# Optimization experiments

Hardware: AMD Instinct MI355X
Metric: run time of the kernel (lower is better)

Reference implementation:

```python
import jax, jax.numpy as jnp
import numpy as np

EPS = 0.05
ITERS = 10


def setup_inputs() -> dict:
    key = jax.random.key(0)
    k1, k2, k3 = jax.random.split(key, 3)
    x = jax.random.normal(k1, (32, 768, 32, 32), jnp.float32)          # [B,C,H,W]
    conv_w = jax.random.normal(k2, (384, 768), jnp.float32) * 0.02     # 1x1 conv kernel [D,C]
    conv_b = jnp.zeros((384,), jnp.float32)
    v = jax.random.normal(k3, (64, 384), jnp.float32)                  # cluster codebook [K,D]
    return {"x": x, "conv_w": conv_w, "conv_b": conv_b, "v": v}


def log_sinkhorn_iterations(Z, log_mu, log_nu, iters):
    # Z: [B,M,N]; log_mu: [B,M]; log_nu: [B,N]
    u0 = jnp.zeros_like(log_mu)
    v0 = jnp.zeros_like(log_nu)

    def step(carry, _):
        u, v = carry
        u = log_mu - jax.nn.logsumexp(Z + v[:, None, :], axis=2)
        v = log_nu - jax.nn.logsumexp(Z + u[:, :, None], axis=1)
        return (u, v), None

    (u, v), _ = jax.lax.scan(step, (u0, v0), None, length=iters)
    return Z + u[:, :, None] + v[:, None, :]


def log_optimal_transport(scores, eps, iters):
    b, m, n = scores.shape
    norm = -jnp.log(jnp.asarray(float(m + n), scores.dtype))
    log_mu = jnp.full((b, m), norm, scores.dtype)
    log_nu = jnp.full((b, n), norm, scores.dtype)
    Z = log_sinkhorn_iterations(scores / eps, log_mu, log_nu, iters)
    return jnp.exp(Z - norm)


def reference(x, conv_w, conv_b, v):
    b, c, h, w = x.shape
    d = conv_w.shape[0]
    # 1x1 conv projection, then flatten spatial and move channels last: [B, HW, D]
    x_proj = jnp.einsum('bchw,dc->bhwd', x, conv_w).reshape(b, h * w, d) + conv_b
    # l2_normalize tokens
    xn = x_proj / jnp.maximum(jnp.linalg.norm(x_proj, axis=-1, keepdims=True), 1e-12)
    # normalized cluster codebook (torch does this under no_grad + in-place copy)
    clusters = v / jnp.maximum(jnp.linalg.norm(v, axis=-1, keepdims=True), 1e-12)  # [K,D]
    # cluster scores: [B, HW, K]
    scores = jnp.einsum('bnd,kd->bnk', xn, clusters)
    # OT on transposed scores [B,K,HW], transpose weights back to [B,HW,K]
    weights = jnp.transpose(
        log_optimal_transport(jnp.transpose(scores, (0, 2, 1)), EPS, ITERS), (0, 2, 1))
    # v_tilde = (x^T @ weights)^T : [B, K, D]
    v_tilde = jnp.einsum('bnd,bnk->bkd', xn, weights)
    return (v_tilde, x_proj)
```

## Files before the change

kernel.cpp:

```cpp
#include <hip/hip_runtime.h>
#include <math.h>

#define BB 32
#define CC 768
#define HWN 1024
#define DD 384
#define KK 64
#define EPSI 20.0f
#define NORMC (-6.9920964f)
#define NITERS 10

typedef __bf16 bf16;
typedef bf16 bf16x8 __attribute__((ext_vector_type(8)));
typedef bf16 bf16x4 __attribute__((ext_vector_type(4)));
typedef float f32x4 __attribute__((ext_vector_type(4)));
typedef _Float16 f16;
typedef f16 f16x2 __attribute__((ext_vector_type(2)));
typedef f16 f16x4 __attribute__((ext_vector_type(4)));

__device__ __forceinline__ float wave_sum(float v){
  #pragma unroll
  for (int off = 32; off; off >>= 1) v += __shfl_xor(v, off, 64);
  return v;
}
__device__ __forceinline__ float wave_max(float v){
  #pragma unroll
  for (int off = 32; off; off >>= 1) v = fmaxf(v, __shfl_xor(v, off, 64));
  return v;
}

__device__ __forceinline__ void async16(const bf16* g, bf16* l){
  __builtin_amdgcn_global_load_lds((const __attribute__((address_space(1))) unsigned int*)g,
                                   (__attribute__((address_space(3))) unsigned int*)l,
                                   16, 0, 0);
}

__global__ __launch_bounds__(256) void k0_clusters(const float* __restrict__ vin,
                                                   bf16* __restrict__ clusb){
  int w = threadIdx.x >> 6, l = threadIdx.x & 63;
  int k = blockIdx.x * 4 + w;
  float s = 0.f;
  #pragma unroll
  for (int i = 0; i < 6; i++){ float x = vin[k*DD + l + 64*i]; s += x*x; }
  s = wave_sum(s);
  float scale = 1.f / fmaxf(sqrtf(s), 1e-12f);
  #pragma unroll
  for (int i = 0; i < 6; i++) clusb[k*DD + l + 64*i] = (bf16)(vin[k*DD + l + 64*i] * scale);
}

__global__ __launch_bounds__(256) void k_wconv(const float* __restrict__ w,
                                               bf16* __restrict__ wb){
  int i = (blockIdx.x * 256 + threadIdx.x) * 4;
  float4 v = *(const float4*)&w[i];
  bf16x4 o;
  o[0] = (bf16)v.x; o[1] = (bf16)v.y; o[2] = (bf16)v.z; o[3] = (bf16)v.w;
  *(bf16x4*)&wb[i] = o;
}

__global__ __launch_bounds__(256) void k_xt(const float* __restrict__ x,
                                            bf16* __restrict__ xt){
  __shared__ float S[64][68];
  int b  = blockIdx.z;
  int k0 = blockIdx.y * 64;
  int n0 = blockIdx.x * 64;
  const float* X = x + (size_t)b * CC * HWN;
  int t = threadIdx.x;
  int rr = t >> 4, cc = (t & 15) * 4;
  #pragma unroll
  for (int it = 0; it < 4; it++){
    float4 v = *(const float4*)&X[(size_t)(k0 + rr + it*16)*HWN + n0 + cc];
    *(float4*)&S[rr + it*16][cc] = v;
  }
  __syncthreads();
  int n = t >> 2, kc = t & 3;
  bf16* orow = xt + (size_t)b * HWN * CC + (size_t)(n0 + n) * CC + k0;
  #pragma unroll
  for (int half = 0; half < 2; half++){
    int kb = half*32 + kc*8;
    bf16x8 o;
    #pragma unroll
    for (int jj = 0; jj < 8; jj++){
      int j = (jj + kc) & 7;
      o[j] = (bf16)S[kb + j][n];
    }
    *(bf16x8*)&orow[kb] = o;
  }
}

__global__ __launch_bounds__(512) void k_gemm(const bf16* __restrict__ Wb,
                                              const bf16* __restrict__ Xt,
                                              const float* __restrict__ bias,
                                              float* __restrict__ xp){
  __shared__ bf16 Wl[384][4][8];
  __shared__ bf16 Xl[128][4][8];
  int b  = blockIdx.y;
  int n0 = blockIdx.x * 128;
  int t = threadIdx.x, wv = t >> 6, l = t & 63;
  int l15 = l & 15, quad = l >> 4;
  int wn = wv >> 2, wm = wv & 3;
  const bf16* Xb = Xt + (size_t)b * HWN * CC;

  int rbase = wv*16 + (l >> 2);
  int kq8   = (l & 3) * 8;
  const bf16* gX = Xb + (size_t)(n0 + rbase) * CC + kq8;
  const bf16* gW = Wb + (size_t)rbase * CC + kq8;
  bf16* lX = &Xl[0][0][0] + wv * 512;
  bf16* lW = &Wl[0][0][0] + wv * 512;

  f32x4 acc[4][6];
  const f32x4 zero = {0.f, 0.f, 0.f, 0.f};
  #pragma unroll
  for (int i = 0; i < 4; i++)
    #pragma unroll
    for (int j = 0; j < 6; j++) acc[i][j] = zero;

  for (int k0 = 0; k0 < CC; k0 += 32){
    async16(gX + k0, lX);
    async16(gW + k0,                  lW);
    async16(gW + k0 + (size_t)128*CC, lW + 4096);
    async16(gW + k0 + (size_t)256*CC, lW + 8192);
    __syncthreads();
    bf16x8 xf[4], wf[6];
    #pragma unroll
    for (int i = 0; i < 4; i++)
      xf[i] = *(const bf16x8*)&Xl[wn*64 + i*16 + l15][quad][0];
    #pragma unroll
    for (int j = 0; j < 6; j++)
      wf[j] = *(const bf16x8*)&Wl[wm*96 + j*16 + l15][quad][0];
    #pragma unroll
    for (int i = 0; i < 4; i++)
      #pragma unroll
      for (int j = 0; j < 6; j++)
        acc[i][j] = __builtin_amdgcn_mfma_f32_16x16x32_bf16(xf[i], wf[j], acc[i][j], 0, 0, 0);
    __syncthreads();
  }

  float bb[6];
  #pragma unroll
  for (int j = 0; j < 6; j++) bb[j] = bias[wm*96 + j*16 + l15];
  #pragma unroll
  for (int i = 0; i < 4; i++){
    int nb = n0 + wn*64 + i*16 + quad*4;
    #pragma unroll
    for (int r = 0; r < 4; r++){
      float* orow = xp + ((size_t)b * HWN + nb + r) * DD;
      #pragma unroll
      for (int j = 0; j < 6; j++)
        orow[wm*96 + j*16 + l15] = acc[i][j][r] + bb[j];
    }
  }
}

__global__ __launch_bounds__(256) void k2_rnorm(const float* __restrict__ xp,
                                                float* __restrict__ rn){
  int w = threadIdx.x >> 6, l = threadIdx.x & 63;
  int t = blockIdx.x * 4 + w;
  const float* row = xp + (size_t)t * DD;
  float s = 0.f;
  #pragma unroll
  for (int i = 0; i < 6; i++){ float xv = row[l + 64*i]; s += xv*xv; }
  s = wave_sum(s);
  if (l == 0) rn[t] = 1.f / fmaxf(sqrtf(s), 1e-12f);
}

__global__ __launch_bounds__(256) void k_xpt(const float* __restrict__ xp,
                                             const float* __restrict__ rn,
                                             bf16* __restrict__ xpt,
                                             bf16* __restrict__ xnb){
  __shared__ float S[64][68];
  int b  = blockIdx.z;
  int d0 = blockIdx.y * 64;
  int n0 = blockIdx.x * 64;
  const float* xpb = xp + (size_t)b * HWN * DD;
  const float* rnb = rn + (size_t)b * HWN;
  int t = threadIdx.x;
  int rr = t >> 4, cc = (t & 15) * 4;
  #pragma unroll
  for (int it = 0; it < 4; it++){
    int row = rr + it*16;
    float sc = rnb[n0 + row];
    float4 v = *(const float4*)&xpb[(size_t)(n0 + row)*DD + d0 + cc];
    v.x *= sc; v.y *= sc; v.z *= sc; v.w *= sc;
    *(float4*)&S[row][cc] = v;
    bf16x4 o4;
    o4[0] = (bf16)v.x; o4[1] = (bf16)v.y; o4[2] = (bf16)v.z; o4[3] = (bf16)v.w;
    *(bf16x4*)&xnb[((size_t)b * HWN + n0 + row)*DD + d0 + cc] = o4;
  }
  __syncthreads();
  int d = t >> 2, c0 = (t & 3) * 16;
  bf16* orow = xpt + (size_t)b * DD * HWN + (size_t)(d0 + d) * HWN + n0 + c0;
  bf16x8 o0, o1;
  #pragma unroll
  for (int jj = 0; jj < 8; jj++) o0[jj] = (bf16)S[c0 + jj][d];
  #pragma unroll
  for (int jj = 0; jj < 8; jj++) o1[jj] = (bf16)S[c0 + 8 + jj][d];
  *(bf16x8*)&orow[0] = o0;
  *(bf16x8*)&orow[8] = o1;
}

__global__ __launch_bounds__(256) void k3_scores(const bf16* __restrict__ clusb,
                                                 const bf16* __restrict__ xnb,
                                                 float* __restrict__ Z){
  __shared__ bf16 Al[64][4][8];
  __shared__ bf16 Bl[128][4][8];
  int b = blockIdx.y, n0 = blockIdx.x * 128;
  const bf16* Xb = xnb + (size_t)b * HWN * DD;
  int t = threadIdx.x, wv = t >> 6, l = t & 63;
  int l15 = l & 15, quad = l >> 4;

  int rbase = wv*16 + (l >> 2);
  int kq8   = (l & 3) * 8;
  const bf16* gA = clusb + (size_t)rbase * DD + kq8;
  const bf16* gB = Xb + (size_t)(n0 + rbase) * DD + kq8;
  bf16* lA = &Al[0][0][0] + wv * 512;
  bf16* lB = &Bl[0][0][0] + wv * 512;

  f32x4 acc[4][2];
  const f32x4 zero = {0.f, 0.f, 0.f, 0.f};
  #pragma unroll
  for (int i = 0; i < 4; i++){ acc[i][0] = zero; acc[i][1] = zero; }

  for (int d0 = 0; d0 < DD; d0 += 32){
    async16(gA + d0, lA);
    async16(gB + d0,                 lB);
    async16(gB + d0 + (size_t)64*DD, lB + 2048);
    __syncthreads();
    bf16x8 af[4], bf[2];
    #pragma unroll
    for (int i = 0; i < 4; i++)
      af[i] = *(const bf16x8*)&Al[i*16 + l15][quad][0];
    #pragma unroll
    for (int j = 0; j < 2; j++)
      bf[j] = *(const bf16x8*)&Bl[wv*32 + j*16 + l15][quad][0];
    #pragma unroll
    for (int i = 0; i < 4; i++)
      #pragma unroll
      for (int j = 0; j < 2; j++)
        acc[i][j] = __builtin_amdgcn_mfma_f32_16x16x32_bf16(af[i], bf[j], acc[i][j], 0, 0, 0);
    __syncthreads();
  }
  #pragma unroll
  for (int i = 0; i < 4; i++){
    #pragma unroll
    for (int j = 0; j < 2; j++){
      int n = n0 + wv*32 + j*16 + l15;
      #pragma unroll
      for (int r = 0; r < 4; r++){
        int k = i*16 + quad*4 + r;
        Z[((size_t)b*KK + k)*HWN + n] = acc[i][j][r] * EPSI;
      }
    }
  }
}

__global__ __launch_bounds__(1024) void k4_sinkhorn(const float* __restrict__ Z,
                                                    float* __restrict__ U,
                                                    float* __restrict__ V){
  __shared__ f16  E[64][1024];
  __shared__ float evf[1024];
  __shared__ float eu[64];
  __shared__ float rmax[64];
  __shared__ float u_l[64];
  __shared__ float v_l[1024];
  __shared__ float sp[2][1024];
  int b = blockIdx.x;
  const float* Zb = Z + (size_t)b * KK * HWN;
  int t = threadIdx.x, w = t >> 6, l = t & 63;

  #pragma unroll
  for (int rr = 0; rr < 4; rr++){
    int r = w*4 + rr;
    float4 z[4];
    float mx = -INFINITY;
    #pragma unroll
    for (int j = 0; j < 4; j++){
      z[j] = *(const float4*)&Zb[(size_t)r*HWN + 4*l + 256*j];
      mx = fmaxf(mx, fmaxf(fmaxf(z[j].x, z[j].y), fmaxf(z[j].z, z[j].w)));
    }
    mx = wave_max(mx);
    if (l == 0) rmax[r] = mx;
    #pragma unroll
    for (int j = 0; j < 4; j++){
      f16x4 e4;
      e4[0] = (f16)__expf(z[j].x - mx); e4[1] = (f16)__expf(z[j].y - mx);
      e4[2] = (f16)__expf(z[j].z - mx); e4[3] = (f16)__expf(z[j].w - mx);
      *(f16x4*)&E[r][4*l + 256*j] = e4;
    }
  }
  evf[t] = 1.f;
  v_l[t] = 0.f;
  __syncthreads();

  for (int it = 0; it < NITERS; it++){
    float evx[16];
    #pragma unroll
    for (int j = 0; j < 8; j++){
      float2 e2 = *(const float2*)&evf[2*(l + 64*j)];
      evx[2*j] = e2.x; evx[2*j+1] = e2.y;
    }
    float us[4];
    #pragma unroll
    for (int rr = 0; rr < 4; rr++){
      int r = w*4 + rr;
      float s = 0.f;
      #pragma unroll
      for (int j = 0; j < 8; j++){
        f16x2 e2 = *(const f16x2*)&E[r][2*(l + 64*j)];
        s = fmaf((float)e2[0], evx[2*j],   s);
        s = fmaf((float)e2[1], evx[2*j+1], s);
      }
      us[rr] = wave_sum(s);
    }
    if (l == 0){
      #pragma unroll
      for (int rr = 0; rr < 4; rr++){
        int r = w*4 + rr;
        u_l[r] = NORMC - rmax[r] - __logf(us[rr]);
        eu[r]  = __expf(NORMC) / us[rr];
      }
    }
    __syncthreads();
    {
      int p = t & 511, h = t >> 9;
      float sx = 0.f, sy = 0.f;
      #pragma unroll
      for (int mq = 0; mq < 8; mq++){
        float4 eu4 = *(const float4*)&eu[h*32 + mq*4];
        const float euv[4] = {eu4.x, eu4.y, eu4.z, eu4.w};
        #pragma unroll
        for (int i = 0; i < 4; i++){
          f16x2 e2 = *(const f16x2*)&E[h*32 + mq*4 + i][2*p];
          sx = fmaf((float)e2[0], euv[i], sx);
          sy = fmaf((float)e2[1], euv[i], sy);
        }
      }
      float2 o; o.x = sx; o.y = sy;
      *(float2*)&sp[h][2*p] = o;
    }
    __syncthreads();
    if (t < 512){
      int p = t;
      float2 a = *(const float2*)&sp[0][2*p];
      float2 c = *(const float2*)&sp[1][2*p];
      float vx = NORMC - __logf(a.x + c.x);
      float vy = NORMC - __logf(a.y + c.y);
      v_l[2*p]   = vx;
      v_l[2*p+1] = vy;
      float2 ee; ee.x = __expf(vx); ee.y = __expf(vy);
      *(float2*)&evf[2*p] = ee;
    }
    __syncthreads();
  }
  V[b*HWN + t] = v_l[t];
  if (t < 64) U[b*KK + t] = u_l[t];
}

__global__ __launch_bounds__(256) void k5_mfma(const float* __restrict__ Z,
                                               const float* __restrict__ U,
                                               const float* __restrict__ V,
                                               const bf16* __restrict__ XpT,
                                               float* __restrict__ out){
  __shared__ bf16 El[64][40];
  __shared__ bf16 Xl[384][40];
  int b  = blockIdx.y;
  int nsb = blockIdx.x * 128;
  const float* Zb = Z + (size_t)b * KK * HWN;
  const bf16*  Xb = XpT + (size_t)b * DD * HWN;
  const float* Vb = V + (size_t)b * HWN;
  int t = threadIdx.x, wv = t >> 6, l = t & 63;
  int l15 = l & 15, quad = l >> 4;
  int er = t >> 2, ec0 = (t & 3) * 8;
  float ur = U[b*KK + er];

  f32x4 acc[4][6];
  const f32x4 zero = {0.f, 0.f, 0.f, 0.f};
  #pragma unroll
  for (int i = 0; i < 4; i++)
    #pragma unroll
    for (int j = 0; j < 6; j++) acc[i][j] = zero;

  for (int st = 0; st < 4; st++){
    int n0 = nsb + st*32;
    {
      float4 z0 = *(const float4*)&Zb[(size_t)er*HWN + n0 + ec0];
      float4 z1 = *(const float4*)&Zb[(size_t)er*HWN + n0 + ec0 + 4];
      float4 v0 = *(const float4*)&Vb[n0 + ec0];
      float4 v1 = *(const float4*)&Vb[n0 + ec0 + 4];
      bf16x8 e;
      e[0] = (bf16)__expf(z0.x + ur + v0.x - NORMC);
      e[1] = (bf16)__expf(z0.y + ur + v0.y - NORMC);
      e[2] = (bf16)__expf(z0.z + ur + v0.z - NORMC);
      e[3] = (bf16)__expf(z0.w + ur + v0.w - NORMC);
      e[4] = (bf16)__expf(z1.x + ur + v1.x - NORMC);
      e[5] = (bf16)__expf(z1.y + ur + v1.y - NORMC);
      e[6] = (bf16)__expf(z1.z + ur + v1.z - NORMC);
      e[7] = (bf16)__expf(z1.w + ur + v1.w - NORMC);
      *(bf16x8*)&El[er][ec0] = e;
    }
    #pragma unroll
    for (int ii = 0; ii < 6; ii++){
      int chunk = t + 256*ii;
      int d = chunk >> 2, cb = (chunk & 3) * 8;
      bf16x8 xv = *(const bf16x8*)&Xb[(size_t)d*HWN + n0 + cb];
      *(bf16x8*)&Xl[d][cb] = xv;
    }
    __syncthreads();
    bf16x8 af[4], bfr[6];
    #pragma unroll
    for (int i = 0; i < 4; i++)
      af[i] = *(const bf16x8*)&El[i*16 + l15][quad*8];
    #pragma unroll
    for (int j = 0; j < 6; j++)
      bfr[j] = *(const bf16x8*)&Xl[wv*96 + j*16 + l15][quad*8];
    #pragma unroll
    for (int i = 0; i < 4; i++)
      #pragma unroll
      for (int j = 0; j < 6; j++)
        acc[i][j] = __builtin_amdgcn_mfma_f32_16x16x32_bf16(af[i], bfr[j], acc[i][j], 0, 0, 0);
    __syncthreads();
  }

  float* ob = out + (size_t)b * KK * DD;
  #pragma unroll
  for (int i = 0; i < 4; i++){
    int kbase = i*16 + quad*4;
    #pragma unroll
    for (int j = 0; j < 6; j++){
      int d = wv*96 + j*16 + l15;
      #pragma unroll
      for (int r = 0; r < 4; r++)
        unsafeAtomicAdd(&ob[(size_t)(kbase + r)*DD + d], acc[i][j][r]);
    }
  }
}

extern "C" void kernel_launch(void* const* d_in, const int* in_sizes, int n_in,
                              void* d_out, int out_size, void* d_ws, size_t ws_size,
                              hipStream_t stream) {
  const float* x      = (const float*)d_in[0];
  const float* conv_w = (const float*)d_in[1];
  const float* conv_b = (const float*)d_in[2];
  const float* vcode  = (const float*)d_in[3];
  float* out = (float*)d_out;
  float* vt_out = out;
  float* xp_out = out + 786432;

  bf16* Xt    = (bf16*)d_ws;
  bf16* Wb    = Xt + (size_t)BB * HWN * CC;
  bf16* clusb = Wb + (size_t)DD * CC;
  float* Zbuf = (float*)(clusb + 24576);
  float* Ubuf = Zbuf + 2097152;
  float* Vbuf = Ubuf + 2048;
  float* Rn   = Vbuf + 32768;
  bf16* xnb   = (bf16*)(Rn + 32768);
  bf16* XpT   = Xt;

  hipMemsetAsync(vt_out, 0, (size_t)786432 * sizeof(float), stream);
  k0_clusters<<<16, 256, 0, stream>>>(vcode, clusb);
  k_wconv<<<288, 256, 0, stream>>>(conv_w, Wb);
  k_xt<<<dim3(16, 12, 32), 256, 0, stream>>>(x, Xt);
  k_gemm<<<dim3(8, 32), 512, 0, stream>>>(Wb, Xt, conv_b, xp_out);
  k2_rnorm<<<8192, 256, 0, stream>>>(xp_out, Rn);
  k_xpt<<<dim3(16, 6, 32), 256, 0, stream>>>(xp_out, Rn, XpT, xnb);
  k3_scores<<<dim3(8, 32), 256, 0, stream>>>(clusb, xnb, Zbuf);
  k4_sinkhorn<<<32, 1024, 0, stream>>>(Zbuf, Ubuf, Vbuf);
  k5_mfma<<<dim3(8, 32), 256, 0, stream>>>(Zbuf, Ubuf, Vbuf, XpT, vt_out);
}
```

Measured before the change: 310.1 us.

## Fuse input transpose and row normalization into projection GEMM

The separate fp32→bf16 transpose of x is dropped. The GEMM now reads fp32 x directly, transposes it through a swizzled shared-memory tile and converts to bf16 inside the K loop. Row L2 norms are computed in the GEMM epilogue with shuffles and a shared reduction, and the normalized bf16 tokens are written there too. This removes the k2_rnorm kernel, and the later transpose now reads bf16 instead of fp32. The X operand loses its async copy and is loaded synchronously with conversion, which may stall the GEMM main loop.

```diff
diff --git a/kernel.cpp b/kernel.cpp
--- a/kernel.cpp
+++ b/kernel.cpp
@@ -57,55 +57,31 @@
   *(bf16x4*)&wb[i] = o;
 }
 
-__global__ __launch_bounds__(256) void k_xt(const float* __restrict__ x,
-                                            bf16* __restrict__ xt){
-  __shared__ float S[64][68];
-  int b  = blockIdx.z;
-  int k0 = blockIdx.y * 64;
-  int n0 = blockIdx.x * 64;
-  const float* X = x + (size_t)b * CC * HWN;
-  int t = threadIdx.x;
-  int rr = t >> 4, cc = (t & 15) * 4;
-  #pragma unroll
-  for (int it = 0; it < 4; it++){
-    float4 v = *(const float4*)&X[(size_t)(k0 + rr + it*16)*HWN + n0 + cc];
-    *(float4*)&S[rr + it*16][cc] = v;
-  }
-  __syncthreads();
-  int n = t >> 2, kc = t & 3;
-  bf16* orow = xt + (size_t)b * HWN * CC + (size_t)(n0 + n) * CC + k0;
-  #pragma unroll
-  for (int half = 0; half < 2; half++){
-    int kb = half*32 + kc*8;
-    bf16x8 o;
-    #pragma unroll
-    for (int jj = 0; jj < 8; jj++){
-      int j = (jj + kc) & 7;
-      o[j] = (bf16)S[kb + j][n];
-    }
-    *(bf16x8*)&orow[kb] = o;
-  }
-}
-
 __global__ __launch_bounds__(512) void k_gemm(const bf16* __restrict__ Wb,
-                                              const bf16* __restrict__ Xt,
+                                              const float* __restrict__ X,
                                               const float* __restrict__ bias,
-                                              float* __restrict__ xp){
-  __shared__ bf16 Wl[384][4][8];
-  __shared__ bf16 Xl[128][4][8];
+                                              float* __restrict__ xp,
+                                              bf16* __restrict__ xnb){
+  __shared__ bf16  Wl[384][4][8];
+  __shared__ float Xf[128 * 36];
+  __shared__ float part[4][128];
+  __shared__ float rn_l[128];
   int b  = blockIdx.y;
   int n0 = blockIdx.x * 128;
   int t = threadIdx.x, wv = t >> 6, l = t & 63;
   int l15 = l & 15, quad = l >> 4;
   int wn = wv >> 2, wm = wv & 3;
-  const bf16* Xb = Xt + (size_t)b * HWN * CC;
+  const float* Xg = X + (size_t)b * CC * HWN;
 
   int rbase = wv*16 + (l >> 2);
   int kq8   = (l & 3) * 8;
-  const bf16* gX = Xb + (size_t)(n0 + rbase) * CC + kq8;
   const bf16* gW = Wb + (size_t)rbase * CC + kq8;
-  bf16* lX = &Xl[0][0][0] + wv * 512;
   bf16* lW = &Wl[0][0][0] + wv * 512;
+
+  int q = t & 31, h = t >> 5;
+  int n4 = q * 4, c2 = h * 2;
+  int sthr = (q ^ (q >> 2)) & 3;
+  int coff = (((c2 >> 3) ^ sthr) << 3) + (c2 & 7);
 
   f32x4 acc[4][6];
   const f32x4 zero = {0.f, 0.f, 0.f, 0.f};
@@ -114,16 +90,40 @@
     #pragma unroll
     for (int j = 0; j < 6; j++) acc[i][j] = zero;
 
-  for (int k0 = 0; k0 < CC; k0 += 32){
-    async16(gX + k0, lX);
-    async16(gW + k0,                  lW);
-    async16(gW + k0 + (size_t)128*CC, lW + 4096);
-    async16(gW + k0 + (size_t)256*CC, lW + 8192);
-    __syncthreads();
+  int a_ = l15 >> 2;
+
+  for (int c0 = 0; c0 < CC; c0 += 32){
+    const float* xr = Xg + (size_t)(c0 + c2) * HWN + n0 + n4;
+    float4 v0 = *(const float4*)xr;
+    float4 v1 = *(const float4*)(xr + HWN);
+    {
+      float2 w0; w0.x = v0.x; w0.y = v1.x;
+      float2 w1; w1.x = v0.y; w1.y = v1.y;
+      float2 w2; w2.x = v0.z; w2.y = v1.z;
+      float2 w3; w3.x = v0.w; w3.y = v1.w;
+      *(float2*)&Xf[(n4+0)*36 + coff] = w0;
+      *(float2*)&Xf[(n4+1)*36 + coff] = w1;
+      *(float2*)&Xf[(n4+2)*36 + coff] = w2;
+      *(float2*)&Xf[(n4+3)*36 + coff] = w3;
+    }
+    async16(gW + c0,                  lW);
+    async16(gW + c0 + (size_t)128*CC, lW + 4096);
+    async16(gW + c0 + (size_t)256*CC, lW + 8192);
+    __syncthreads();
+
     bf16x8 xf[4], wf[6];
     #pragma unroll
-    for (int i = 0; i < 4; i++)
-      xf[i] = *(const bf16x8*)&Xl[wn*64 + i*16 + l15][quad][0];
+    for (int i = 0; i < 4; i++){
+      int nloc = wn*64 + i*16 + l15;
+      int s = (a_ ^ (wn*4 + i)) & 3;
+      int blk = quad ^ s;
+      const float4 f0 = *(const float4*)&Xf[nloc*36 + blk*8];
+      const float4 f1 = *(const float4*)&Xf[nloc*36 + blk*8 + 4];
+      bf16x8 xv;
+      xv[0] = (bf16)f0.x; xv[1] = (bf16)f0.y; xv[2] = (bf16)f0.z; xv[3] = (bf16)f0.w;
+      xv[4] = (bf16)f1.x; xv[5] = (bf16)f1.y; xv[6] = (bf16)f1.z; xv[7] = (bf16)f1.w;
+      xf[i] = xv;
+    }
     #pragma unroll
     for (int j = 0; j < 6; j++)
       wf[j] = *(const bf16x8*)&Wl[wm*96 + j*16 + l15][quad][0];
@@ -138,62 +138,67 @@
   float bb[6];
   #pragma unroll
   for (int j = 0; j < 6; j++) bb[j] = bias[wm*96 + j*16 + l15];
+
   #pragma unroll
   for (int i = 0; i < 4; i++){
-    int nb = n0 + wn*64 + i*16 + quad*4;
     #pragma unroll
     for (int r = 0; r < 4; r++){
-      float* orow = xp + ((size_t)b * HWN + nb + r) * DD;
-      #pragma unroll
-      for (int j = 0; j < 6; j++)
-        orow[wm*96 + j*16 + l15] = acc[i][j][r] + bb[j];
-    }
-  }
-}
-
-__global__ __launch_bounds__(256) void k2_rnorm(const float* __restrict__ xp,
-                                                float* __restrict__ rn){
-  int w = threadIdx.x >> 6, l = threadIdx.x & 63;
-  int t = blockIdx.x * 4 + w;
-  const float* row = xp + (size_t)t * DD;
-  float s = 0.f;
-  #pragma unroll
-  for (int i = 0; i < 6; i++){ float xv = row[l + 64*i]; s += xv*xv; }
-  s = wave_sum(s);
-  if (l == 0) rn[t] = 1.f / fmaxf(sqrtf(s), 1e-12f);
-}
-
-__global__ __launch_bounds__(256) void k_xpt(const float* __restrict__ xp,
-                                             const float* __restrict__ rn,
-                                             bf16* __restrict__ xpt,
-                                             bf16* __restrict__ xnb){
-  __shared__ float S[64][68];
+      float s = 0.f;
+      #pragma unroll
+      for (int j = 0; j < 6; j++){ float v = acc[i][j][r] + bb[j]; s = fmaf(v, v, s); }
+      s += __shfl_xor(s, 1, 64); s += __shfl_xor(s, 2, 64);
+      s += __shfl_xor(s, 4, 64); s += __shfl_xor(s, 8, 64);
+      if (l15 == 0) part[wm][wn*64 + i*16 + quad*4 + r] = s;
+    }
+  }
+  __syncthreads();
+  if (t < 128){
+    float tot = part[0][t] + part[1][t] + part[2][t] + part[3][t];
+    rn_l[t] = 1.f / fmaxf(sqrtf(tot), 1e-12f);
+  }
+  __syncthreads();
+
+  #pragma unroll
+  for (int i = 0; i < 4; i++){
+    #pragma unroll
+    for (int r = 0; r < 4; r++){
+      int nloc = wn*64 + i*16 + quad*4 + r;
+      float rv = rn_l[nloc];
+      float* orow = xp  + ((size_t)b * HWN + n0 + nloc) * DD;
+      bf16*  xrow = xnb + ((size_t)b * HWN + n0 + nloc) * DD;
+      #pragma unroll
+      for (int j = 0; j < 6; j++){
+        int m = wm*96 + j*16 + l15;
+        float val = acc[i][j][r] + bb[j];
+        orow[m] = val;
+        xrow[m] = (bf16)(val * rv);
+      }
+    }
+  }
+}
+
+__global__ __launch_bounds__(256) void k_xpt2(const bf16* __restrict__ xnb,
+                                              bf16* __restrict__ xpt){
+  __shared__ bf16 S[64][72];
   int b  = blockIdx.z;
   int d0 = blockIdx.y * 64;
   int n0 = blockIdx.x * 64;
-  const float* xpb = xp + (size_t)b * HWN * DD;
-  const float* rnb = rn + (size_t)b * HWN;
+  const bf16* src = xnb + ((size_t)b * HWN + n0) * DD + d0;
   int t = threadIdx.x;
-  int rr = t >> 4, cc = (t & 15) * 4;
-  #pragma unroll
-  for (int it = 0; it < 4; it++){
-    int row = rr + it*16;
-    float sc = rnb[n0 + row];
-    float4 v = *(const float4*)&xpb[(size_t)(n0 + row)*DD + d0 + cc];
-    v.x *= sc; v.y *= sc; v.z *= sc; v.w *= sc;
-    *(float4*)&S[row][cc] = v;
-    bf16x4 o4;
-    o4[0] = (bf16)v.x; o4[1] = (bf16)v.y; o4[2] = (bf16)v.z; o4[3] = (bf16)v.w;
-    *(bf16x4*)&xnb[((size_t)b * HWN + n0 + row)*DD + d0 + cc] = o4;
+  int r = t >> 3, c8 = (t & 7) * 8;
+  #pragma unroll
+  for (int it = 0; it < 2; it++){
+    bf16x8 v = *(const bf16x8*)&src[(size_t)(r + it*32) * DD + c8];
+    *(bf16x8*)&S[r + it*32][c8] = v;
   }
   __syncthreads();
   int d = t >> 2, c0 = (t & 3) * 16;
-  bf16* orow = xpt + (size_t)b * DD * HWN + (size_t)(d0 + d) * HWN + n0 + c0;
+  bf16* orow = xpt + ((size_t)b * DD + d0 + d) * HWN + n0 + c0;
   bf16x8 o0, o1;
   #pragma unroll
-  for (int jj = 0; jj < 8; jj++) o0[jj] = (bf16)S[c0 + jj][d];
-  #pragma unroll
-  for (int jj = 0; jj < 8; jj++) o1[jj] = (bf16)S[c0 + 8 + jj][d];
+  for (int jj = 0; jj < 8; jj++) o0[jj] = S[c0 + jj][d];
+  #pragma unroll
+  for (int jj = 0; jj < 8; jj++) o1[jj] = S[c0 + 8 + jj][d];
   *(bf16x8*)&orow[0] = o0;
   *(bf16x8*)&orow[8] = o1;
 }
@@ -445,23 +450,19 @@
   float* vt_out = out;
   float* xp_out = out + 786432;
 
-  bf16* Xt    = (bf16*)d_ws;
-  bf16* Wb    = Xt + (size_t)BB * HWN * CC;
+  bf16* xnb   = (bf16*)d_ws;
+  bf16* XpT   = xnb + (size_t)BB * HWN * DD;
+  bf16* Wb    = XpT + (size_t)BB * HWN * DD;
   bf16* clusb = Wb + (size_t)DD * CC;
   float* Zbuf = (float*)(clusb + 24576);
   float* Ubuf = Zbuf + 2097152;
   float* Vbuf = Ubuf + 2048;
-  float* Rn   = Vbuf + 32768;
-  bf16* xnb   = (bf16*)(Rn + 32768);
-  bf16* XpT   = Xt;
 
   hipMemsetAsync(vt_out, 0, (size_t)786432 * sizeof(float), stream);
   k0_clusters<<<16, 256, 0, stream>>>(vcode, clusb);
   k_wconv<<<288, 256, 0, stream>>>(conv_w, Wb);
-  k_xt<<<dim3(16, 12, 32), 256, 0, stream>>>(x, Xt);
-  k_gemm<<<dim3(8, 32), 512, 0, stream>>>(Wb, Xt, conv_b, xp_out);
-  k2_rnorm<<<8192, 256, 0, stream>>>(xp_out, Rn);
-  k_xpt<<<dim3(16, 6, 32), 256, 0, stream>>>(xp_out, Rn, XpT, xnb);
+  k_gemm<<<dim3(8, 32), 512, 0, stream>>>(Wb, x, conv_b, xp_out, xnb);
+  k_xpt2<<<dim3(16, 6, 32), 256, 0, stream>>>(xnb, XpT);
   k3_scores<<<dim3(8, 32), 256, 0, stream>>>(clusb, xnb, Zbuf);
   k4_sinkhorn<<<32, 1024, 0, stream>>>(Zbuf, Ubuf, Vbuf);
   k5_mfma<<<dim3(8, 32), 256, 0, stream>>>(Zbuf, Ubuf, Vbuf, XpT, vt_out);
```

Result: faster. 295.9 us (-4.6%).
